# Kernel tuning notes

Measured on AMD Instinct MI355X. Metric: run time of the kernel, lower is better.

Reference implementation:

```python
import jax, jax.numpy as jnp
import numpy as np

NUM_HEADS = 8
LN_EPS = 1e-5


def setup_inputs() -> dict:
    key = jax.random.key(0)
    ks = jax.random.split(key, 9)
    B, C, H, W = 8, 512, 32, 32
    s = 1.0 / np.sqrt(C)
    return {
        "f_curr": jax.random.normal(ks[0], (B, C, H, W), dtype=jnp.float32),
        "f_prev": jax.random.normal(ks[1], (B, C, H, W), dtype=jnp.float32),
        "f_next": jax.random.normal(ks[2], (B, C, H, W), dtype=jnp.float32),
        "Wq": jax.random.normal(ks[3], (C, C), dtype=jnp.float32) * s,
        "Wk": jax.random.normal(ks[4], (C, C), dtype=jnp.float32) * s,
        "Wv": jax.random.normal(ks[5], (C, C), dtype=jnp.float32) * s,
        "Wo": jax.random.normal(ks[6], (C, C), dtype=jnp.float32) * s,
        "gamma": jnp.ones((C,), dtype=jnp.float32),
        "beta": jnp.zeros((C,), dtype=jnp.float32),
    }


def _flatten(f):
    # [B,C,H,W] -> [B, H*W, C]
    B, C, H, W = f.shape
    return f.reshape(B, C, H * W).transpose(0, 2, 1)


def reference(f_curr, f_prev, f_next, Wq, Wk, Wv, Wo, gamma, beta):
    B, C, H, W = f_curr.shape
    N = H * W
    hd = C // NUM_HEADS
    scale = hd ** -0.5

    curr_flat = _flatten(f_curr)                              # [B,N,C]
    neigh_flat = jnp.concatenate([_flatten(f_prev), _flatten(f_next)], axis=1)  # [B,2N,C]

    # torch Linear (no bias): y = x @ W.T
    Q = curr_flat @ Wq.T                                      # [B,N,C]
    K = neigh_flat @ Wk.T                                     # [B,2N,C]
    V = neigh_flat @ Wv.T                                     # [B,2N,C]

    def split_heads(t, L):
        return t.reshape(B, L, NUM_HEADS, hd).transpose(0, 2, 1, 3)  # [B,h,L,hd]

    Qh = split_heads(Q, N)
    Kh = split_heads(K, 2 * N)
    Vh = split_heads(V, 2 * N)

    scores = jnp.einsum("bhnd,bhmd->bhnm", Qh, Kh) * scale    # [B,h,N,2N]
    attn = jax.nn.softmax(scores, axis=-1)
    out = jnp.einsum("bhnm,bhmd->bhnd", attn, Vh)             # [B,h,N,hd]

    out = out.transpose(0, 2, 1, 3).reshape(B, N, C)          # merge heads
    out = curr_flat + out @ Wo.T                              # residual

    # LayerNorm over channel dim
    mu = jnp.mean(out, axis=-1, keepdims=True)
    var = jnp.mean(jnp.square(out - mu), axis=-1, keepdims=True)
    out = (out - mu) * jax.lax.rsqrt(var + LN_EPS) * gamma + beta

    return out.transpose(0, 2, 1).reshape(B, C, H, W)
```

## Files before the change

kernel.cpp:

```cpp
#include <hip/hip_runtime.h>
#include <hip/hip_bf16.h>
#include <math.h>

#define NH 8
#define HD 64
#define CH 512
#define NT 1024
#define NB 8

typedef __bf16 bf16_t;
typedef bf16_t bf16x8 __attribute__((ext_vector_type(8)));
typedef bf16_t bf16x4 __attribute__((ext_vector_type(4)));
typedef float  f32x4  __attribute__((ext_vector_type(4)));
typedef float  f32x16 __attribute__((ext_vector_type(16)));

#define MFMA16(a, b, c) __builtin_amdgcn_mfma_f32_16x16x32_bf16((a), (b), (c), 0, 0, 0)
#define MFMA32(a, b, c) __builtin_amdgcn_mfma_f32_32x32x16_bf16((a), (b), (c), 0, 0, 0)

__device__ __forceinline__ void gload16(const void* g, void* l) {
    __builtin_amdgcn_global_load_lds(
        (const __attribute__((address_space(1))) void*)g,
        (__attribute__((address_space(3))) void*)l, 16, 0, 0);
}

__global__ __launch_bounds__(256) void prep_kernel(
    const float* __restrict__ fc, const float* __restrict__ fp,
    const float* __restrict__ fn, bf16_t* __restrict__ Xc,
    bf16_t* __restrict__ Xn)
{
    __shared__ __align__(16) bf16_t tile[64 * 64];
    const int t = threadIdx.x;
    const int y = blockIdx.y;
    const int b = y / 3, ft = y % 3;
    const int c0 = (blockIdx.x & 7) * 64;
    const int n0 = (blockIdx.x >> 3) * 64;

    const float* src; bf16_t* dst;
    if (ft == 0)      { src = fc + (size_t)b * CH * NT; dst = Xc + (size_t)b * NT * CH; }
    else if (ft == 1) { src = fp + (size_t)b * CH * NT; dst = Xn + (size_t)b * 2 * NT * CH; }
    else              { src = fn + (size_t)b * CH * NT; dst = Xn + (size_t)b * 2 * NT * CH + (size_t)NT * CH; }

    const int nb = t & 15, cb = t >> 4;
    float4 ld[4];
#pragma unroll
    for (int i = 0; i < 4; ++i)
        ld[i] = *(const float4*)(src + (size_t)(c0 + cb * 4 + i) * NT + n0 + nb * 4);
    const float* lf = (const float*)ld;
#pragma unroll
    for (int j = 0; j < 4; ++j) {
        int n = nb * 4 + j;
        int v = (n >> 2) & 14;
        bf16x4 wv = { (bf16_t)lf[0 * 4 + j], (bf16_t)lf[1 * 4 + j],
                      (bf16_t)lf[2 * 4 + j], (bf16_t)lf[3 * 4 + j] };
        *(bf16x4*)(tile + n * 64 + ((cb ^ v) * 4)) = wv;
    }
    __syncthreads();
#pragma unroll
    for (int i = 0; i < 2; ++i) {
        int gid = t + i * 256;
        int n = gid >> 3, c16 = gid & 7;
        int v = (n >> 2) & 14;
        bf16x8 val = *(const bf16x8*)(tile + n * 64 + (((2 * c16) ^ v) * 4));
        *(bf16x8*)(dst + (size_t)(n0 + n) * CH + c0 + c16 * 8) = val;
    }
}

__global__ __launch_bounds__(256) void wcvt_kernel(
    const float* __restrict__ Wq, const float* __restrict__ Wk,
    const float* __restrict__ Wv, const float* __restrict__ Wo,
    bf16_t* __restrict__ Wb)
{
    const int m = blockIdx.y;
    const float* src = (m == 0) ? Wq : (m == 1) ? Wk : (m == 2) ? Wv : Wo;
    bf16_t* dst = Wb + (size_t)m * CH * CH;
    int gid = blockIdx.x * 256 + threadIdx.x;
    float4 v = *(const float4*)(src + (size_t)gid * 4);
    bf16x4 o = { (bf16_t)v.x, (bf16_t)v.y, (bf16_t)v.z, (bf16_t)v.w };
    *(bf16x4*)(dst + (size_t)gid * 4) = o;
}

template <bool SWAP>
__device__ __forceinline__ void gemm_core(const bf16_t* __restrict__ A,
                                          const bf16_t* __restrict__ B,
                                          bf16_t* aT, bf16_t* bT,
                                          f32x4 acc[4][4])
{
    const int t = threadIdx.x, w = t >> 6, lane = t & 63;
    const int lid = lane & 15, quad = lane >> 4;
    const int wm = w >> 1, wn = w & 1;
    const int l4 = lane >> 2, k4 = lane & 3;

    for (int kt = 0; kt < 16; ++kt) {
        const int k0 = kt * 32;
        __syncthreads();
#pragma unroll
        for (int i = 0; i < 2; ++i) {
            int q = w * 2 + i;
            int row = q * 16 + l4;
            int kk = k4 ^ ((row >> 1) & 3);
            gload16(A + (size_t)row * CH + k0 + kk * 8, aT + q * 512);
            gload16(B + (size_t)row * CH + k0 + kk * 8, bT + q * 512);
        }
        __syncthreads();

        const bf16_t* mT = SWAP ? bT : aT;
        const bf16_t* nT = SWAP ? aT : bT;
        bf16x8 mf[4], nf[4];
#pragma unroll
        for (int i = 0; i < 4; ++i) {
            int row = wm * 64 + i * 16 + lid;
            int kw = quad ^ ((row >> 1) & 3);
            mf[i] = *(const bf16x8*)(mT + row * 32 + kw * 8);
        }
#pragma unroll
        for (int i = 0; i < 4; ++i) {
            int row = wn * 64 + i * 16 + lid;
            int kw = quad ^ ((row >> 1) & 3);
            nf[i] = *(const bf16x8*)(nT + row * 32 + kw * 8);
        }
#pragma unroll
        for (int mi = 0; mi < 4; ++mi)
#pragma unroll
            for (int ni = 0; ni < 4; ++ni)
                acc[mi][ni] = MFMA16(mf[mi], nf[ni], acc[mi][ni]);
    }
}

__global__ __launch_bounds__(256) void qkv_kernel(
    const bf16_t* __restrict__ Xc, const bf16_t* __restrict__ Xn,
    const bf16_t* __restrict__ Wb,
    bf16_t* __restrict__ Qn, bf16_t* __restrict__ Kn, bf16_t* __restrict__ Vt)
{
    __shared__ __align__(16) bf16_t aT[128 * 32];
    __shared__ __align__(16) bf16_t bT[128 * 32];
    const int bx = blockIdx.x, b = blockIdx.y;
    const int t = threadIdx.x, w = t >> 6, lane = t & 63;
    const int lid = lane & 15, quad = lane >> 4;
    const int wm = w >> 1, wn = w & 1;
    const float QSC = 0.125f * 1.44269504f;

    f32x4 acc[4][4] = {};

    if (bx < 96) {
        const bf16_t* A; const bf16_t* B; bf16_t* O; float scale;
        if (bx < 32) {
            int nt = bx >> 2, ct = bx & 3;
            A = Xc + (size_t)b * NT * CH + (size_t)nt * 128 * CH;
            B = Wb + (size_t)0 * CH * CH + (size_t)ct * 128 * CH;
            O = Qn + (size_t)b * NT * CH + (size_t)nt * 128 * CH + ct * 128;
            scale = QSC;
        } else {
            int j = bx - 32, nt = j >> 2, ct = j & 3;
            A = Xn + (size_t)b * 2 * NT * CH + (size_t)nt * 128 * CH;
            B = Wb + (size_t)1 * CH * CH + (size_t)ct * 128 * CH;
            O = Kn + (size_t)b * 2 * NT * CH + (size_t)nt * 128 * CH + ct * 128;
            scale = 1.0f;
        }
        gemm_core<false>(A, B, aT, bT, acc);
#pragma unroll
        for (int mi = 0; mi < 4; ++mi)
#pragma unroll
            for (int ni = 0; ni < 4; ++ni)
#pragma unroll
                for (int r = 0; r < 4; ++r) {
                    int n  = wm * 64 + mi * 16 + quad * 4 + r;
                    int co = wn * 64 + ni * 16 + lid;
                    O[(size_t)n * CH + co] = (bf16_t)(acc[mi][ni][r] * scale);
                }
    } else {
        int j = bx - 96, nt = j >> 2, ct = j & 3;
        const bf16_t* A = Xn + (size_t)b * 2 * NT * CH + (size_t)nt * 128 * CH;
        const bf16_t* B = Wb + (size_t)2 * CH * CH + (size_t)ct * 128 * CH;
        bf16_t* O = Vt + (size_t)b * CH * 2 * NT + (size_t)ct * 128 * 2 * NT + nt * 128;
        gemm_core<true>(A, B, aT, bT, acc);
#pragma unroll
        for (int mi = 0; mi < 4; ++mi)
#pragma unroll
            for (int ni = 0; ni < 4; ++ni)
#pragma unroll
                for (int r = 0; r < 4; ++r) {
                    int co_l  = wm * 64 + mi * 16 + quad * 4 + r;
                    int key_l = wn * 64 + ni * 16 + lid;
                    O[(size_t)co_l * (2 * NT) + key_l] = (bf16_t)acc[mi][ni][r];
                }
    }
}

__global__ __launch_bounds__(256) void attn_kernel(
    const bf16_t* __restrict__ Qn, const bf16_t* __restrict__ Kn,
    const bf16_t* __restrict__ Vt, bf16_t* __restrict__ AOn)
{
    __shared__ __align__(16) bf16_t kv[128 * 72];
    __shared__ __align__(16) float  pqf[9216];
    __shared__ float l_scr[128];

    bf16_t* pq = (bf16_t*)pqf;

    const int t = threadIdx.x;
    const int w = t >> 6, lane = t & 63;
    const int wq = w >> 1, wk = w & 1;
    const int l31 = lane & 31, h = lane >> 5;

    const int q0 = blockIdx.x * 128;
    const int hh = blockIdx.y, b = blockIdx.z;

    const bf16_t* Qb  = Qn + ((size_t)b * NT + q0) * CH + hh * HD;
    const bf16_t* Kb  = Kn + (size_t)b * 2 * NT * CH + hh * HD;
    const bf16_t* Vtb = Vt + ((size_t)b * CH + hh * HD) * (2 * NT);
    bf16_t* AOb = AOn + ((size_t)b * NT + q0) * CH + hh * HD;

#pragma unroll
    for (int i = 0; i < 4; ++i) {
        int gid = t + i * 256;
        int qr = gid >> 3, c8 = (gid & 7) * 8;
        *(bf16x8*)(pq + qr * 72 + (c8 ^ (qr & 24))) =
            *(const bf16x8*)(Qb + (size_t)qr * CH + c8);
    }
    __syncthreads();

    bf16x8 kreg[4];
#pragma unroll
    for (int i = 0; i < 4; ++i) {
        int gid = t + i * 256;
        int kr = gid >> 3, c8 = (gid & 7) * 8;
        kreg[i] = *(const bf16x8*)(Kb + (size_t)kr * CH + c8);
    }

    bf16x8 qf[2][4];
#pragma unroll
    for (int nf = 0; nf < 2; ++nf)
#pragma unroll
        for (int ks = 0; ks < 4; ++ks) {
            int row = wq * 64 + nf * 32 + l31;
            int col = (ks * 16 + h * 8) ^ (row & 24);
            qf[nf][ks] = *(const bf16x8*)(pq + row * 72 + col);
        }
    __syncthreads();

    bf16_t* pw = pq + w * 4608;

    f32x16 o[2][2] = {};
    float lpart[2] = {0.f, 0.f};

    for (int kt = 0; kt < 16; ++kt) {
        const int kbase = kt * 128;

#pragma unroll
        for (int i = 0; i < 4; ++i) {
            int gid = t + i * 256;
            int kr = gid >> 3, c8 = (gid & 7) * 8;
            *(bf16x8*)(kv + kr * 72 + (c8 ^ (kr & 24))) = kreg[i];
        }
        __syncthreads();

        bf16x8 vreg[4];
#pragma unroll
        for (int i = 0; i < 4; ++i) {
            int gid = t + i * 256;
            int dr = gid >> 4, c8 = (gid & 15) * 8;
            vreg[i] = *(const bf16x8*)(Vtb + (size_t)dr * (2 * NT) + kbase + c8);
        }

        f32x16 s[2][2] = {};
#pragma unroll
        for (int ks = 0; ks < 4; ++ks) {
            bf16x8 af[2];
#pragma unroll
            for (int mf = 0; mf < 2; ++mf) {
                int arow = wk * 64 + mf * 32 + l31;
                int acol = (ks * 16 + h * 8) ^ (arow & 24);
                af[mf] = *(const bf16x8*)(kv + arow * 72 + acol);
            }
#pragma unroll
            for (int mf = 0; mf < 2; ++mf)
#pragma unroll
                for (int nf = 0; nf < 2; ++nf)
                    s[mf][nf] = MFMA32(af[mf], qf[nf][ks], s[mf][nf]);
        }

#pragma unroll
        for (int mf = 0; mf < 2; ++mf)
#pragma unroll
            for (int nf = 0; nf < 2; ++nf) {
                int qrow = nf * 32 + l31;
#pragma unroll
                for (int g = 0; g < 4; ++g) {
                    float p0 = exp2f(s[mf][nf][4 * g + 0]);
                    float p1 = exp2f(s[mf][nf][4 * g + 1]);
                    float p2 = exp2f(s[mf][nf][4 * g + 2]);
                    float p3 = exp2f(s[mf][nf][4 * g + 3]);
                    lpart[nf] += (p0 + p1) + (p2 + p3);
                    bf16x4 pk = { (bf16_t)p0, (bf16_t)p1, (bf16_t)p2, (bf16_t)p3 };
                    int kb = mf * 32 + 8 * g + 4 * h;
                    *(bf16x4*)(pw + qrow * 72 + (kb ^ (qrow & 24))) = pk;
                }
            }
        __syncthreads();

#pragma unroll
        for (int i = 0; i < 4; ++i) {
            int gid = t + i * 256;
            int dr = gid >> 4, c8 = (gid & 15) * 8;
            *(bf16x8*)(kv + dr * 136 + (c8 ^ (dr & 24))) = vreg[i];
        }
        __syncthreads();

        const int nb2 = (kt < 15) ? kbase + 128 : kbase;
#pragma unroll
        for (int i = 0; i < 4; ++i) {
            int gid = t + i * 256;
            int kr = gid >> 3, c8 = (gid & 7) * 8;
            kreg[i] = *(const bf16x8*)(Kb + (size_t)(nb2 + kr) * CH + c8);
        }

#pragma unroll
        for (int ks = 0; ks < 4; ++ks) {
            bf16x8 av[2], bp[2];
#pragma unroll
            for (int df = 0; df < 2; ++df) {
                int vrow = df * 32 + l31;
                int vcol = (wk * 64 + ks * 16 + h * 8) ^ (vrow & 24);
                av[df] = *(const bf16x8*)(kv + vrow * 136 + vcol);
            }
#pragma unroll
            for (int nf = 0; nf < 2; ++nf) {
                int bq = nf * 32 + l31;
                int bcol = (ks * 16 + h * 8) ^ (bq & 24);
                bp[nf] = *(const bf16x8*)(pw + bq * 72 + bcol);
            }
#pragma unroll
            for (int df = 0; df < 2; ++df)
#pragma unroll
                for (int nf = 0; nf < 2; ++nf)
                    o[df][nf] = MFMA32(av[df], bp[nf], o[df][nf]);
        }
        __syncthreads();
    }

    float l2[2];
#pragma unroll
    for (int nf = 0; nf < 2; ++nf)
        l2[nf] = lpart[nf] + __shfl_xor(lpart[nf], 32);

    if (wk == 1) {
        float* scr = pqf + wq * 4352;
#pragma unroll
        for (int df = 0; df < 2; ++df)
#pragma unroll
            for (int nf = 0; nf < 2; ++nf) {
                int qrow = nf * 32 + l31;
#pragma unroll
                for (int g = 0; g < 4; ++g) {
                    int d = df * 32 + 8 * g + 4 * h;
                    f32x4 v = { o[df][nf][4 * g + 0], o[df][nf][4 * g + 1],
                                o[df][nf][4 * g + 2], o[df][nf][4 * g + 3] };
                    *(f32x4*)(scr + qrow * 68 + d) = v;
                }
            }
        if (h == 0) {
            l_scr[wq * 64 + 0 * 32 + l31] = l2[0];
            l_scr[wq * 64 + 1 * 32 + l31] = l2[1];
        }
    }
    __syncthreads();

    if (wk == 0) {
        const float* scr = pqf + wq * 4352;
        float inv[2];
#pragma unroll
        for (int nf = 0; nf < 2; ++nf)
            inv[nf] = 1.0f / (l2[nf] + l_scr[wq * 64 + nf * 32 + l31]);
#pragma unroll
        for (int df = 0; df < 2; ++df)
#pragma unroll
            for (int nf = 0; nf < 2; ++nf) {
                int qrow = nf * 32 + l31;
#pragma unroll
                for (int g = 0; g < 4; ++g) {
                    int d = df * 32 + 8 * g + 4 * h;
                    f32x4 part = *(const f32x4*)(scr + qrow * 68 + d);
                    bf16x4 ov = {
                        (bf16_t)((o[df][nf][4 * g + 0] + part.x) * inv[nf]),
                        (bf16_t)((o[df][nf][4 * g + 1] + part.y) * inv[nf]),
                        (bf16_t)((o[df][nf][4 * g + 2] + part.z) * inv[nf]),
                        (bf16_t)((o[df][nf][4 * g + 3] + part.w) * inv[nf]) };
                    int qg = wq * 64 + qrow;
                    *(bf16x4*)(kv + qg * 72 + (d ^ (qg & 24))) = ov;
                }
            }
    }
    __syncthreads();

#pragma unroll
    for (int i = 0; i < 4; ++i) {
        int gid = t + i * 256;
        int qr = gid >> 3, c8 = (gid & 7) * 8;
        *(bf16x8*)(AOb + (size_t)qr * CH + c8) =
            *(const bf16x8*)(kv + qr * 72 + (c8 ^ (qr & 24)));
    }
}

__global__ __launch_bounds__(256) void proj_kernel(
    const bf16_t* __restrict__ AOn, const bf16_t* __restrict__ Wb,
    const float* __restrict__ fc, float* __restrict__ Zt)
{
    __shared__ __align__(16) bf16_t aT[128 * 32];
    __shared__ __align__(16) bf16_t bT[128 * 32];
    const int bx = blockIdx.x, b = blockIdx.y;
    const int nt = bx >> 2, ct = bx & 3;
    const int t = threadIdx.x, w = t >> 6, lane = t & 63;
    const int lid = lane & 15, quad = lane >> 4;
    const int wm = w >> 1, wn = w & 1;

    const bf16_t* A = AOn + (size_t)b * NT * CH + (size_t)nt * 128 * CH;
    const bf16_t* B = Wb + (size_t)3 * CH * CH + (size_t)ct * 128 * CH;

    f32x4 acc[4][4] = {};
    gemm_core<true>(A, B, aT, bT, acc);

    const size_t bofs = (size_t)b * CH * NT;
#pragma unroll
    for (int mi = 0; mi < 4; ++mi)
#pragma unroll
        for (int ni = 0; ni < 4; ++ni)
#pragma unroll
            for (int r = 0; r < 4; ++r) {
                int co_l = wm * 64 + mi * 16 + quad * 4 + r;
                int n_l  = wn * 64 + ni * 16 + lid;
                size_t idx = bofs + (size_t)(ct * 128 + co_l) * NT + nt * 128 + n_l;
                Zt[idx] = acc[mi][ni][r] + fc[idx];
            }
}

__global__ __launch_bounds__(256) void stats_kernel(
    const float* __restrict__ Zt, float* __restrict__ mu_buf,
    float* __restrict__ rs_buf)
{
    __shared__ float sS[1024], sQ[1024];
    const int b = blockIdx.y, n0 = blockIdx.x * 64;
    const int t = threadIdx.x, w = t >> 6, lane = t & 63;
    const int co_off = lane >> 4, n4 = lane & 15;
    const float* Zb = Zt + (size_t)b * CH * NT + n0 + n4 * 4;

    f32x4 s = {0, 0, 0, 0}, q = {0, 0, 0, 0};
    for (int it = 0; it < 32; ++it) {
        int co = w * 4 + co_off + it * 16;
        f32x4 z = *(const f32x4*)(Zb + (size_t)co * NT);
#pragma unroll
        for (int c = 0; c < 4; ++c) { s[c] += z[c]; q[c] += z[c] * z[c]; }
    }
#pragma unroll
    for (int c = 0; c < 4; ++c) { sS[t * 4 + c] = s[c]; sQ[t * 4 + c] = q[c]; }
    __syncthreads();

    if (t < 64) {
        int n4r = t >> 2, comp = t & 3;
        float ss = 0.f, qq = 0.f;
#pragma unroll
        for (int i = 0; i < 16; ++i) {
            int idx = ((i >> 2) * 64 + (i & 3) * 16 + n4r) * 4 + comp;
            ss += sS[idx]; qq += sQ[idx];
        }
        float mu  = ss * (1.0f / 512.0f);
        float var = qq * (1.0f / 512.0f) - mu * mu;
        mu_buf[(size_t)b * NT + n0 + t] = mu;
        rs_buf[(size_t)b * NT + n0 + t] = rsqrtf(var + 1e-5f);
    }
}

__global__ __launch_bounds__(256) void apply_kernel(
    const float* __restrict__ Zt, const float* __restrict__ mu_buf,
    const float* __restrict__ rs_buf, const float* __restrict__ gamma,
    const float* __restrict__ beta, float* __restrict__ out)
{
    const int row = blockIdx.x;
    const int co = row & 511, b = row >> 9;
    const int t = threadIdx.x;
    const float g = gamma[co], be = beta[co];
    const size_t base = (size_t)row * NT + t * 4;
    f32x4 z  = *(const f32x4*)(Zt + base);
    f32x4 mu = *(const f32x4*)(mu_buf + (size_t)b * NT + t * 4);
    f32x4 rs = *(const f32x4*)(rs_buf + (size_t)b * NT + t * 4);
    f32x4 o;
#pragma unroll
    for (int c = 0; c < 4; ++c) o[c] = (z[c] - mu[c]) * rs[c] * g + be;
    *(f32x4*)(out + base) = o;
}

extern "C" void kernel_launch(void* const* d_in, const int* in_sizes, int n_in,
                              void* d_out, int out_size, void* d_ws, size_t ws_size,
                              hipStream_t stream)
{
    (void)in_sizes; (void)n_in; (void)out_size; (void)ws_size;
    const float* fc    = (const float*)d_in[0];
    const float* fp    = (const float*)d_in[1];
    const float* fn    = (const float*)d_in[2];
    const float* Wq    = (const float*)d_in[3];
    const float* Wk    = (const float*)d_in[4];
    const float* Wv    = (const float*)d_in[5];
    const float* Wo    = (const float*)d_in[6];
    const float* gamma = (const float*)d_in[7];
    const float* beta  = (const float*)d_in[8];
    float* out = (float*)d_out;

    char* ws = (char*)d_ws;
    bf16_t* Xn  = (bf16_t*)(ws);
    bf16_t* Qn  = (bf16_t*)(ws + 16777216);
    bf16_t* Kn  = (bf16_t*)(ws + 25165824);
    bf16_t* Xc  = (bf16_t*)(ws + 41943040);
    bf16_t* AOn = Xc;
    bf16_t* Vt  = (bf16_t*)(ws + 50331648);
    bf16_t* Wb  = (bf16_t*)(ws + 67108864);
    float*  mu  = (float*)(ws + 69206016);
    float*  rs  = (float*)(ws + 69238784);
    float*  Zt  = (float*)(ws);

    prep_kernel<<<dim3(128, 24), 256, 0, stream>>>(fc, fp, fn, Xc, Xn);
    wcvt_kernel<<<dim3(256, 4), 256, 0, stream>>>(Wq, Wk, Wv, Wo, Wb);
    qkv_kernel<<<dim3(160, 8), 256, 0, stream>>>(Xc, Xn, Wb, Qn, Kn, Vt);
    attn_kernel<<<dim3(8, 8, 8), 256, 0, stream>>>(Qn, Kn, Vt, AOn);
    proj_kernel<<<dim3(32, 8), 256, 0, stream>>>(AOn, Wb, fc, Zt);
    stats_kernel<<<dim3(16, 8), 256, 0, stream>>>(Zt, mu, rs);
    apply_kernel<<<4096, 256, 0, stream>>>(Zt, mu, rs, gamma, beta, out);
}
```

Measured before the change: 252.9 us.

## Restructure attention K/V staging, use raw exp, fuse LayerNorm stats and apply

The attention kernel now gives K and V their own LDS buffers. Both are prefetched one tile ahead into registers and stored together, which cuts the per-iteration barriers from four to two. The XOR swizzle is replaced with an additive skew, and exp2f is replaced by an inline v_exp_f32 to avoid range-handling code. The separate stats and apply kernels are merged into one LayerNorm kernel that reads Zt twice but skips the mu/rs round trip and one launch. The fused LN kernel uses only 128 blocks with scalar strided loads, so it may use bandwidth poorly. The extra LDS buffer may also lower attention occupancy.

```diff
diff --git a/kernel.cpp b/kernel.cpp
--- a/kernel.cpp
+++ b/kernel.cpp
@@ -17,10 +17,18 @@
 #define MFMA16(a, b, c) __builtin_amdgcn_mfma_f32_16x16x32_bf16((a), (b), (c), 0, 0, 0)
 #define MFMA32(a, b, c) __builtin_amdgcn_mfma_f32_32x32x16_bf16((a), (b), (c), 0, 0, 0)
 
+#define SKW(r) (((r) >> 2) & 6)
+
 __device__ __forceinline__ void gload16(const void* g, void* l) {
     __builtin_amdgcn_global_load_lds(
         (const __attribute__((address_space(1))) void*)g,
         (__attribute__((address_space(3))) void*)l, 16, 0, 0);
+}
+
+__device__ __forceinline__ float fexp2(float x) {
+    float r;
+    asm("v_exp_f32 %0, %1" : "=v"(r) : "v"(x));
+    return r;
 }
 
 __global__ __launch_bounds__(256) void prep_kernel(
@@ -190,10 +198,10 @@
     const bf16_t* __restrict__ Qn, const bf16_t* __restrict__ Kn,
     const bf16_t* __restrict__ Vt, bf16_t* __restrict__ AOn)
 {
-    __shared__ __align__(16) bf16_t kv[128 * 72];
+    __shared__ __align__(16) bf16_t k_lds[128 * 72];
+    __shared__ __align__(16) bf16_t v_lds[64 * 136];
     __shared__ __align__(16) float  pqf[9216];
     __shared__ float l_scr[128];
-
     bf16_t* pq = (bf16_t*)pqf;
 
     const int t = threadIdx.x;
@@ -209,22 +217,16 @@
     const bf16_t* Vtb = Vt + ((size_t)b * CH + hh * HD) * (2 * NT);
     bf16_t* AOb = AOn + ((size_t)b * NT + q0) * CH + hh * HD;
 
-#pragma unroll
-    for (int i = 0; i < 4; ++i) {
-        int gid = t + i * 256;
-        int qr = gid >> 3, c8 = (gid & 7) * 8;
-        *(bf16x8*)(pq + qr * 72 + (c8 ^ (qr & 24))) =
-            *(const bf16x8*)(Qb + (size_t)qr * CH + c8);
-    }
-    __syncthreads();
-
-    bf16x8 kreg[4];
-#pragma unroll
-    for (int i = 0; i < 4; ++i) {
-        int gid = t + i * 256;
-        int kr = gid >> 3, c8 = (gid & 7) * 8;
-        kreg[i] = *(const bf16x8*)(Kb + (size_t)kr * CH + c8);
-    }
+    {
+        int qr = t >> 3, c8 = (t & 7) * 8;
+#pragma unroll
+        for (int i = 0; i < 4; ++i) {
+            int row = qr + i * 32;
+            *(bf16x8*)(pq + row * 72 + c8 + SKW(row)) =
+                *(const bf16x8*)(Qb + (size_t)row * CH + c8);
+        }
+    }
+    __syncthreads();
 
     bf16x8 qf[2][4];
 #pragma unroll
@@ -232,33 +234,47 @@
 #pragma unroll
         for (int ks = 0; ks < 4; ++ks) {
             int row = wq * 64 + nf * 32 + l31;
-            int col = (ks * 16 + h * 8) ^ (row & 24);
-            qf[nf][ks] = *(const bf16x8*)(pq + row * 72 + col);
+            qf[nf][ks] = *(const bf16x8*)(pq + row * 72 + ks * 16 + h * 8 + SKW(row));
         }
     __syncthreads();
 
     bf16_t* pw = pq + w * 4608;
+
+    const int kr0 = t >> 3, kc8 = (t & 7) * 8;
+    const int dr0 = t >> 4, vc8 = (t & 15) * 8;
+    const bf16_t* kg = Kb + (size_t)kr0 * CH + kc8;
+    const bf16_t* vg = Vtb + (size_t)dr0 * (2 * NT) + vc8;
+
+    bf16x8 kreg[4], vreg[4];
+#pragma unroll
+    for (int i = 0; i < 4; ++i) kreg[i] = *(const bf16x8*)(kg + (size_t)i * 32 * CH);
+#pragma unroll
+    for (int i = 0; i < 4; ++i) vreg[i] = *(const bf16x8*)(vg + (size_t)i * 16 * (2 * NT));
+    kg += (size_t)128 * CH; vg += 128;
 
     f32x16 o[2][2] = {};
     float lpart[2] = {0.f, 0.f};
 
     for (int kt = 0; kt < 16; ++kt) {
-        const int kbase = kt * 128;
-
+        __syncthreads();
 #pragma unroll
         for (int i = 0; i < 4; ++i) {
-            int gid = t + i * 256;
-            int kr = gid >> 3, c8 = (gid & 7) * 8;
-            *(bf16x8*)(kv + kr * 72 + (c8 ^ (kr & 24))) = kreg[i];
+            int row = kr0 + i * 32;
+            *(bf16x8*)(k_lds + row * 72 + kc8 + SKW(row)) = kreg[i];
+        }
+#pragma unroll
+        for (int i = 0; i < 4; ++i) {
+            int row = dr0 + i * 16;
+            *(bf16x8*)(v_lds + row * 136 + vc8 + SKW(row)) = vreg[i];
         }
         __syncthreads();
 
-        bf16x8 vreg[4];
-#pragma unroll
-        for (int i = 0; i < 4; ++i) {
-            int gid = t + i * 256;
-            int dr = gid >> 4, c8 = (gid & 15) * 8;
-            vreg[i] = *(const bf16x8*)(Vtb + (size_t)dr * (2 * NT) + kbase + c8);
+        if (kt != 15) {
+#pragma unroll
+            for (int i = 0; i < 4; ++i) kreg[i] = *(const bf16x8*)(kg + (size_t)i * 32 * CH);
+#pragma unroll
+            for (int i = 0; i < 4; ++i) vreg[i] = *(const bf16x8*)(vg + (size_t)i * 16 * (2 * NT));
+            kg += (size_t)128 * CH; vg += 128;
         }
 
         f32x16 s[2][2] = {};
@@ -268,8 +284,7 @@
 #pragma unroll
             for (int mf = 0; mf < 2; ++mf) {
                 int arow = wk * 64 + mf * 32 + l31;
-                int acol = (ks * 16 + h * 8) ^ (arow & 24);
-                af[mf] = *(const bf16x8*)(kv + arow * 72 + acol);
+                af[mf] = *(const bf16x8*)(k_lds + arow * 72 + ks * 16 + h * 8 + SKW(arow));
             }
 #pragma unroll
             for (int mf = 0; mf < 2; ++mf)
@@ -285,33 +300,16 @@
                 int qrow = nf * 32 + l31;
 #pragma unroll
                 for (int g = 0; g < 4; ++g) {
-                    float p0 = exp2f(s[mf][nf][4 * g + 0]);
-                    float p1 = exp2f(s[mf][nf][4 * g + 1]);
-                    float p2 = exp2f(s[mf][nf][4 * g + 2]);
-                    float p3 = exp2f(s[mf][nf][4 * g + 3]);
+                    float p0 = fexp2(s[mf][nf][4 * g + 0]);
+                    float p1 = fexp2(s[mf][nf][4 * g + 1]);
+                    float p2 = fexp2(s[mf][nf][4 * g + 2]);
+                    float p3 = fexp2(s[mf][nf][4 * g + 3]);
                     lpart[nf] += (p0 + p1) + (p2 + p3);
                     bf16x4 pk = { (bf16_t)p0, (bf16_t)p1, (bf16_t)p2, (bf16_t)p3 };
                     int kb = mf * 32 + 8 * g + 4 * h;
-                    *(bf16x4*)(pw + qrow * 72 + (kb ^ (qrow & 24))) = pk;
+                    *(bf16x4*)(pw + qrow * 72 + kb + SKW(qrow)) = pk;
                 }
             }
-        __syncthreads();
-
-#pragma unroll
-        for (int i = 0; i < 4; ++i) {
-            int gid = t + i * 256;
-            int dr = gid >> 4, c8 = (gid & 15) * 8;
-            *(bf16x8*)(kv + dr * 136 + (c8 ^ (dr & 24))) = vreg[i];
-        }
-        __syncthreads();
-
-        const int nb2 = (kt < 15) ? kbase + 128 : kbase;
-#pragma unroll
-        for (int i = 0; i < 4; ++i) {
-            int gid = t + i * 256;
-            int kr = gid >> 3, c8 = (gid & 7) * 8;
-            kreg[i] = *(const bf16x8*)(Kb + (size_t)(nb2 + kr) * CH + c8);
-        }
 
 #pragma unroll
         for (int ks = 0; ks < 4; ++ks) {
@@ -319,14 +317,12 @@
 #pragma unroll
             for (int df = 0; df < 2; ++df) {
                 int vrow = df * 32 + l31;
-                int vcol = (wk * 64 + ks * 16 + h * 8) ^ (vrow & 24);
-                av[df] = *(const bf16x8*)(kv + vrow * 136 + vcol);
+                av[df] = *(const bf16x8*)(v_lds + vrow * 136 + wk * 64 + ks * 16 + h * 8 + SKW(vrow));
             }
 #pragma unroll
             for (int nf = 0; nf < 2; ++nf) {
                 int bq = nf * 32 + l31;
-                int bcol = (ks * 16 + h * 8) ^ (bq & 24);
-                bp[nf] = *(const bf16x8*)(pw + bq * 72 + bcol);
+                bp[nf] = *(const bf16x8*)(pw + bq * 72 + ks * 16 + h * 8 + SKW(bq));
             }
 #pragma unroll
             for (int df = 0; df < 2; ++df)
@@ -334,8 +330,8 @@
                 for (int nf = 0; nf < 2; ++nf)
                     o[df][nf] = MFMA32(av[df], bp[nf], o[df][nf]);
         }
-        __syncthreads();
-    }
+    }
+    __syncthreads();
 
     float l2[2];
 #pragma unroll
@@ -385,18 +381,20 @@
                         (bf16_t)((o[df][nf][4 * g + 2] + part.z) * inv[nf]),
                         (bf16_t)((o[df][nf][4 * g + 3] + part.w) * inv[nf]) };
                     int qg = wq * 64 + qrow;
-                    *(bf16x4*)(kv + qg * 72 + (d ^ (qg & 24))) = ov;
+                    *(bf16x4*)(k_lds + qg * 72 + d + SKW(qg)) = ov;
                 }
             }
     }
     __syncthreads();
 
-#pragma unroll
-    for (int i = 0; i < 4; ++i) {
-        int gid = t + i * 256;
-        int qr = gid >> 3, c8 = (gid & 7) * 8;
-        *(bf16x8*)(AOb + (size_t)qr * CH + c8) =
-            *(const bf16x8*)(kv + qr * 72 + (c8 ^ (qr & 24)));
+    {
+        int qr = t >> 3, c8 = (t & 7) * 8;
+#pragma unroll
+        for (int i = 0; i < 4; ++i) {
+            int row = qr + i * 32;
+            *(bf16x8*)(AOb + (size_t)row * CH + c8) =
+                *(const bf16x8*)(k_lds + row * 72 + c8 + SKW(row));
+        }
     }
 }
 
@@ -432,59 +430,45 @@
             }
 }
 
-__global__ __launch_bounds__(256) void stats_kernel(
-    const float* __restrict__ Zt, float* __restrict__ mu_buf,
-    float* __restrict__ rs_buf)
-{
-    __shared__ float sS[1024], sQ[1024];
+__global__ __launch_bounds__(256) void ln2_kernel(
+    const float* __restrict__ Zt, const float* __restrict__ gamma,
+    const float* __restrict__ beta, float* __restrict__ out)
+{
+    __shared__ float pS[256], pQ[256];
+    __shared__ float mu_s[64], rs_s[64];
     const int b = blockIdx.y, n0 = blockIdx.x * 64;
-    const int t = threadIdx.x, w = t >> 6, lane = t & 63;
-    const int co_off = lane >> 4, n4 = lane & 15;
-    const float* Zb = Zt + (size_t)b * CH * NT + n0 + n4 * 4;
-
-    f32x4 s = {0, 0, 0, 0}, q = {0, 0, 0, 0};
-    for (int it = 0; it < 32; ++it) {
-        int co = w * 4 + co_off + it * 16;
-        f32x4 z = *(const f32x4*)(Zb + (size_t)co * NT);
-#pragma unroll
-        for (int c = 0; c < 4; ++c) { s[c] += z[c]; q[c] += z[c] * z[c]; }
-    }
-#pragma unroll
-    for (int c = 0; c < 4; ++c) { sS[t * 4 + c] = s[c]; sQ[t * 4 + c] = q[c]; }
-    __syncthreads();
-
+    const int t = threadIdx.x;
+    const int n = t & 63, cg = t >> 6;
+    const float* Zb = Zt + (size_t)b * CH * NT + n0 + n;
+
+    float s = 0.f, q = 0.f;
+#pragma unroll 8
+    for (int k = 0; k < 128; ++k) {
+        int co = cg * 128 + k;
+        float z = Zb[(size_t)co * NT];
+        s += z; q += z * z;
+    }
+    pS[cg * 64 + n] = s; pQ[cg * 64 + n] = q;
+    __syncthreads();
     if (t < 64) {
-        int n4r = t >> 2, comp = t & 3;
         float ss = 0.f, qq = 0.f;
 #pragma unroll
-        for (int i = 0; i < 16; ++i) {
-            int idx = ((i >> 2) * 64 + (i & 3) * 16 + n4r) * 4 + comp;
-            ss += sS[idx]; qq += sQ[idx];
-        }
+        for (int i = 0; i < 4; ++i) { ss += pS[i * 64 + t]; qq += pQ[i * 64 + t]; }
         float mu  = ss * (1.0f / 512.0f);
         float var = qq * (1.0f / 512.0f) - mu * mu;
-        mu_buf[(size_t)b * NT + n0 + t] = mu;
-        rs_buf[(size_t)b * NT + n0 + t] = rsqrtf(var + 1e-5f);
-    }
-}
-
-__global__ __launch_bounds__(256) void apply_kernel(
-    const float* __restrict__ Zt, const float* __restrict__ mu_buf,
-    const float* __restrict__ rs_buf, const float* __restrict__ gamma,
-    const float* __restrict__ beta, float* __restrict__ out)
-{
-    const int row = blockIdx.x;
-    const int co = row & 511, b = row >> 9;
-    const int t = threadIdx.x;
-    const float g = gamma[co], be = beta[co];
-    const size_t base = (size_t)row * NT + t * 4;
-    f32x4 z  = *(const f32x4*)(Zt + base);
-    f32x4 mu = *(const f32x4*)(mu_buf + (size_t)b * NT + t * 4);
-    f32x4 rs = *(const f32x4*)(rs_buf + (size_t)b * NT + t * 4);
-    f32x4 o;
-#pragma unroll
-    for (int c = 0; c < 4; ++c) o[c] = (z[c] - mu[c]) * rs[c] * g + be;
-    *(f32x4*)(out + base) = o;
+        mu_s[t] = mu;
+        rs_s[t] = rsqrtf(var + 1e-5f);
+    }
+    __syncthreads();
+
+    const float mu = mu_s[n], rs = rs_s[n];
+    float* ob = out + (size_t)b * CH * NT + n0 + n;
+#pragma unroll 8
+    for (int k = 0; k < 128; ++k) {
+        int co = cg * 128 + k;
+        float z = Zb[(size_t)co * NT];
+        ob[(size_t)co * NT] = (z - mu) * rs * gamma[co] + beta[co];
+    }
 }
 
 extern "C" void kernel_launch(void* const* d_in, const int* in_sizes, int n_in,
@@ -511,8 +495,6 @@
     bf16_t* AOn = Xc;
     bf16_t* Vt  = (bf16_t*)(ws + 50331648);
     bf16_t* Wb  = (bf16_t*)(ws + 67108864);
-    float*  mu  = (float*)(ws + 69206016);
-    float*  rs  = (float*)(ws + 69238784);
     float*  Zt  = (float*)(ws);
 
     prep_kernel<<<dim3(128, 24), 256, 0, stream>>>(fc, fp, fn, Xc, Xn);
@@ -520,6 +502,5 @@
     qkv_kernel<<<dim3(160, 8), 256, 0, stream>>>(Xc, Xn, Wb, Qn, Kn, Vt);
     attn_kernel<<<dim3(8, 8, 8), 256, 0, stream>>>(Qn, Kn, Vt, AOn);
     proj_kernel<<<dim3(32, 8), 256, 0, stream>>>(AOn, Wb, fc, Zt);
-    stats_kernel<<<dim3(16, 8), 256, 0, stream>>>(Zt, mu, rs);
-    apply_kernel<<<4096, 256, 0, stream>>>(Zt, mu, rs, gamma, beta, out);
-}
+    ln2_kernel<<<dim3(16, 8), 256, 0, stream>>>(Zt, gamma, beta, out);
+}
```

Measured after the change: 311.3 us. 23.1% more time.

## Widen GEMM tiles to 128x256 and fuse LayerNorm stats with apply

Applied to the files above, without the earlier changes.

The QKV and output-projection GEMMs now use 128x256 tiles, so each block loads a wider slice of the weight matrix and keeps 32 accumulators per thread. This halves the block count and the re-reads of activation tiles. The separate LayerNorm stats and apply kernels are merged into one kernel that computes per-position mean and rstd, then normalizes in a second pass over the same Zt columns. This removes a launch and the mu/rs round trip. The trade-offs are more register pressure, fewer blocks (128 for proj, 128 for LN) leaving many CUs idle on a 256-CU part, and scalar strided loads in the LN kernel.

```diff
diff --git a/kernel.cpp b/kernel.cpp
--- a/kernel.cpp
+++ b/kernel.cpp
@@ -80,11 +80,13 @@
 }
 
 template <bool SWAP>
-__device__ __forceinline__ void gemm_core(const bf16_t* __restrict__ A,
-                                          const bf16_t* __restrict__ B,
-                                          bf16_t* aT, bf16_t* bT,
-                                          f32x4 acc[4][4])
-{
+__device__ __forceinline__ void gemm_core2(const bf16_t* __restrict__ A,
+                                           const bf16_t* __restrict__ B,
+                                           bf16_t* aT, bf16_t* bT,
+                                           f32x4* acc)
+{
+    constexpr int MC = SWAP ? 8 : 4;
+    constexpr int NC = SWAP ? 4 : 8;
     const int t = threadIdx.x, w = t >> 6, lane = t & 63;
     const int lid = lane & 15, quad = lane >> 4;
     const int wm = w >> 1, wn = w & 1;
@@ -99,30 +101,36 @@
             int row = q * 16 + l4;
             int kk = k4 ^ ((row >> 1) & 3);
             gload16(A + (size_t)row * CH + k0 + kk * 8, aT + q * 512);
+        }
+#pragma unroll
+        for (int i = 0; i < 4; ++i) {
+            int q = w * 4 + i;
+            int row = q * 16 + l4;
+            int kk = k4 ^ ((row >> 1) & 3);
             gload16(B + (size_t)row * CH + k0 + kk * 8, bT + q * 512);
         }
         __syncthreads();
 
         const bf16_t* mT = SWAP ? bT : aT;
         const bf16_t* nT = SWAP ? aT : bT;
-        bf16x8 mf[4], nf[4];
-#pragma unroll
-        for (int i = 0; i < 4; ++i) {
-            int row = wm * 64 + i * 16 + lid;
+        bf16x8 mf[MC], nf[NC];
+#pragma unroll
+        for (int i = 0; i < MC; ++i) {
+            int row = wm * (MC * 16) + i * 16 + lid;
             int kw = quad ^ ((row >> 1) & 3);
             mf[i] = *(const bf16x8*)(mT + row * 32 + kw * 8);
         }
 #pragma unroll
-        for (int i = 0; i < 4; ++i) {
-            int row = wn * 64 + i * 16 + lid;
+        for (int i = 0; i < NC; ++i) {
+            int row = wn * (NC * 16) + i * 16 + lid;
             int kw = quad ^ ((row >> 1) & 3);
             nf[i] = *(const bf16x8*)(nT + row * 32 + kw * 8);
         }
 #pragma unroll
-        for (int mi = 0; mi < 4; ++mi)
-#pragma unroll
-            for (int ni = 0; ni < 4; ++ni)
-                acc[mi][ni] = MFMA16(mf[mi], nf[ni], acc[mi][ni]);
+        for (int mi = 0; mi < MC; ++mi)
+#pragma unroll
+            for (int ni = 0; ni < NC; ++ni)
+                acc[mi * NC + ni] = MFMA16(mf[mi], nf[ni], acc[mi * NC + ni]);
     }
 }
 
@@ -132,56 +140,58 @@
     bf16_t* __restrict__ Qn, bf16_t* __restrict__ Kn, bf16_t* __restrict__ Vt)
 {
     __shared__ __align__(16) bf16_t aT[128 * 32];
-    __shared__ __align__(16) bf16_t bT[128 * 32];
+    __shared__ __align__(16) bf16_t bT[256 * 32];
     const int bx = blockIdx.x, b = blockIdx.y;
     const int t = threadIdx.x, w = t >> 6, lane = t & 63;
     const int lid = lane & 15, quad = lane >> 4;
     const int wm = w >> 1, wn = w & 1;
     const float QSC = 0.125f * 1.44269504f;
 
-    f32x4 acc[4][4] = {};
-
-    if (bx < 96) {
+    f32x4 acc[32];
+#pragma unroll
+    for (int i = 0; i < 32; ++i) acc[i] = f32x4{0.f, 0.f, 0.f, 0.f};
+
+    if (bx < 48) {
         const bf16_t* A; const bf16_t* B; bf16_t* O; float scale;
-        if (bx < 32) {
-            int nt = bx >> 2, ct = bx & 3;
+        if (bx < 16) {
+            int nt = bx >> 1, cp = bx & 1;
             A = Xc + (size_t)b * NT * CH + (size_t)nt * 128 * CH;
-            B = Wb + (size_t)0 * CH * CH + (size_t)ct * 128 * CH;
-            O = Qn + (size_t)b * NT * CH + (size_t)nt * 128 * CH + ct * 128;
+            B = Wb + (size_t)0 * CH * CH + (size_t)cp * 256 * CH;
+            O = Qn + (size_t)b * NT * CH + (size_t)nt * 128 * CH + cp * 256;
             scale = QSC;
         } else {
-            int j = bx - 32, nt = j >> 2, ct = j & 3;
+            int j = bx - 16, nt = j >> 1, cp = j & 1;
             A = Xn + (size_t)b * 2 * NT * CH + (size_t)nt * 128 * CH;
-            B = Wb + (size_t)1 * CH * CH + (size_t)ct * 128 * CH;
-            O = Kn + (size_t)b * 2 * NT * CH + (size_t)nt * 128 * CH + ct * 128;
+            B = Wb + (size_t)1 * CH * CH + (size_t)cp * 256 * CH;
+            O = Kn + (size_t)b * 2 * NT * CH + (size_t)nt * 128 * CH + cp * 256;
             scale = 1.0f;
         }
-        gemm_core<false>(A, B, aT, bT, acc);
+        gemm_core2<false>(A, B, aT, bT, acc);
 #pragma unroll
         for (int mi = 0; mi < 4; ++mi)
 #pragma unroll
-            for (int ni = 0; ni < 4; ++ni)
+            for (int ni = 0; ni < 8; ++ni)
 #pragma unroll
                 for (int r = 0; r < 4; ++r) {
                     int n  = wm * 64 + mi * 16 + quad * 4 + r;
-                    int co = wn * 64 + ni * 16 + lid;
-                    O[(size_t)n * CH + co] = (bf16_t)(acc[mi][ni][r] * scale);
+                    int co = wn * 128 + ni * 16 + lid;
+                    O[(size_t)n * CH + co] = (bf16_t)(acc[mi * 8 + ni][r] * scale);
                 }
     } else {
-        int j = bx - 96, nt = j >> 2, ct = j & 3;
+        int j = bx - 48, nt = j >> 1, cp = j & 1;
         const bf16_t* A = Xn + (size_t)b * 2 * NT * CH + (size_t)nt * 128 * CH;
-        const bf16_t* B = Wb + (size_t)2 * CH * CH + (size_t)ct * 128 * CH;
-        bf16_t* O = Vt + (size_t)b * CH * 2 * NT + (size_t)ct * 128 * 2 * NT + nt * 128;
-        gemm_core<true>(A, B, aT, bT, acc);
-#pragma unroll
-        for (int mi = 0; mi < 4; ++mi)
+        const bf16_t* B = Wb + (size_t)2 * CH * CH + (size_t)cp * 256 * CH;
+        bf16_t* O = Vt + (size_t)b * CH * 2 * NT + (size_t)cp * 256 * 2 * NT + nt * 128;
+        gemm_core2<true>(A, B, aT, bT, acc);
+#pragma unroll
+        for (int mi = 0; mi < 8; ++mi)
 #pragma unroll
             for (int ni = 0; ni < 4; ++ni)
 #pragma unroll
                 for (int r = 0; r < 4; ++r) {
-                    int co_l  = wm * 64 + mi * 16 + quad * 4 + r;
+                    int co_l  = wm * 128 + mi * 16 + quad * 4 + r;
                     int key_l = wn * 64 + ni * 16 + lid;
-                    O[(size_t)co_l * (2 * NT) + key_l] = (bf16_t)acc[mi][ni][r];
+                    O[(size_t)co_l * (2 * NT) + key_l] = (bf16_t)acc[mi * 4 + ni][r];
                 }
     }
 }
@@ -405,86 +415,74 @@
     const float* __restrict__ fc, float* __restrict__ Zt)
 {
     __shared__ __align__(16) bf16_t aT[128 * 32];
-    __shared__ __align__(16) bf16_t bT[128 * 32];
+    __shared__ __align__(16) bf16_t bT[256 * 32];
     const int bx = blockIdx.x, b = blockIdx.y;
-    const int nt = bx >> 2, ct = bx & 3;
+    const int nt = bx >> 1, cp = bx & 1;
     const int t = threadIdx.x, w = t >> 6, lane = t & 63;
     const int lid = lane & 15, quad = lane >> 4;
     const int wm = w >> 1, wn = w & 1;
 
     const bf16_t* A = AOn + (size_t)b * NT * CH + (size_t)nt * 128 * CH;
-    const bf16_t* B = Wb + (size_t)3 * CH * CH + (size_t)ct * 128 * CH;
-
-    f32x4 acc[4][4] = {};
-    gemm_core<true>(A, B, aT, bT, acc);
+    const bf16_t* B = Wb + (size_t)3 * CH * CH + (size_t)cp * 256 * CH;
+
+    f32x4 acc[32];
+#pragma unroll
+    for (int i = 0; i < 32; ++i) acc[i] = f32x4{0.f, 0.f, 0.f, 0.f};
+    gemm_core2<true>(A, B, aT, bT, acc);
 
     const size_t bofs = (size_t)b * CH * NT;
 #pragma unroll
-    for (int mi = 0; mi < 4; ++mi)
+    for (int mi = 0; mi < 8; ++mi)
 #pragma unroll
         for (int ni = 0; ni < 4; ++ni)
 #pragma unroll
             for (int r = 0; r < 4; ++r) {
-                int co_l = wm * 64 + mi * 16 + quad * 4 + r;
+                int co_l = wm * 128 + mi * 16 + quad * 4 + r;
                 int n_l  = wn * 64 + ni * 16 + lid;
-                size_t idx = bofs + (size_t)(ct * 128 + co_l) * NT + nt * 128 + n_l;
-                Zt[idx] = acc[mi][ni][r] + fc[idx];
-            }
-}
-
-__global__ __launch_bounds__(256) void stats_kernel(
-    const float* __restrict__ Zt, float* __restrict__ mu_buf,
-    float* __restrict__ rs_buf)
-{
-    __shared__ float sS[1024], sQ[1024];
+                size_t idx = bofs + (size_t)(cp * 256 + co_l) * NT + nt * 128 + n_l;
+                Zt[idx] = acc[mi * 4 + ni][r] + fc[idx];
+            }
+}
+
+__global__ __launch_bounds__(256) void ln2_kernel(
+    const float* __restrict__ Zt, const float* __restrict__ gamma,
+    const float* __restrict__ beta, float* __restrict__ out)
+{
+    __shared__ float pS[256], pQ[256];
+    __shared__ float mu_s[64], rs_s[64];
     const int b = blockIdx.y, n0 = blockIdx.x * 64;
-    const int t = threadIdx.x, w = t >> 6, lane = t & 63;
-    const int co_off = lane >> 4, n4 = lane & 15;
-    const float* Zb = Zt + (size_t)b * CH * NT + n0 + n4 * 4;
-
-    f32x4 s = {0, 0, 0, 0}, q = {0, 0, 0, 0};
-    for (int it = 0; it < 32; ++it) {
-        int co = w * 4 + co_off + it * 16;
-        f32x4 z = *(const f32x4*)(Zb + (size_t)co * NT);
-#pragma unroll
-        for (int c = 0; c < 4; ++c) { s[c] += z[c]; q[c] += z[c] * z[c]; }
-    }
-#pragma unroll
-    for (int c = 0; c < 4; ++c) { sS[t * 4 + c] = s[c]; sQ[t * 4 + c] = q[c]; }
-    __syncthreads();
-
+    const int t = threadIdx.x;
+    const int n = t & 63, cg = t >> 6;
+    const float* Zb = Zt + (size_t)b * CH * NT + n0 + n;
+
+    float s = 0.f, q = 0.f;
+#pragma unroll 8
+    for (int k = 0; k < 128; ++k) {
+        int co = cg * 128 + k;
+        float z = Zb[(size_t)co * NT];
+        s += z; q += z * z;
+    }
+    pS[cg * 64 + n] = s; pQ[cg * 64 + n] = q;
+    __syncthreads();
     if (t < 64) {
-        int n4r = t >> 2, comp = t & 3;
         float ss = 0.f, qq = 0.f;
 #pragma unroll
-        for (int i = 0; i < 16; ++i) {
-            int idx = ((i >> 2) * 64 + (i & 3) * 16 + n4r) * 4 + comp;
-            ss += sS[idx]; qq += sQ[idx];
-        }
+        for (int i = 0; i < 4; ++i) { ss += pS[i * 64 + t]; qq += pQ[i * 64 + t]; }
         float mu  = ss * (1.0f / 512.0f);
         float var = qq * (1.0f / 512.0f) - mu * mu;
-        mu_buf[(size_t)b * NT + n0 + t] = mu;
-        rs_buf[(size_t)b * NT + n0 + t] = rsqrtf(var + 1e-5f);
-    }
-}
-
-__global__ __launch_bounds__(256) void apply_kernel(
-    const float* __restrict__ Zt, const float* __restrict__ mu_buf,
-    const float* __restrict__ rs_buf, const float* __restrict__ gamma,
-    const float* __restrict__ beta, float* __restrict__ out)
-{
-    const int row = blockIdx.x;
-    const int co = row & 511, b = row >> 9;
-    const int t = threadIdx.x;
-    const float g = gamma[co], be = beta[co];
-    const size_t base = (size_t)row * NT + t * 4;
-    f32x4 z  = *(const f32x4*)(Zt + base);
-    f32x4 mu = *(const f32x4*)(mu_buf + (size_t)b * NT + t * 4);
-    f32x4 rs = *(const f32x4*)(rs_buf + (size_t)b * NT + t * 4);
-    f32x4 o;
-#pragma unroll
-    for (int c = 0; c < 4; ++c) o[c] = (z[c] - mu[c]) * rs[c] * g + be;
-    *(f32x4*)(out + base) = o;
+        mu_s[t] = mu;
+        rs_s[t] = rsqrtf(var + 1e-5f);
+    }
+    __syncthreads();
+
+    const float mu = mu_s[n], rs = rs_s[n];
+    float* ob = out + (size_t)b * CH * NT + n0 + n;
+#pragma unroll 8
+    for (int k = 0; k < 128; ++k) {
+        int co = cg * 128 + k;
+        float z = Zb[(size_t)co * NT];
+        ob[(size_t)co * NT] = (z - mu) * rs * gamma[co] + beta[co];
+    }
 }
 
 extern "C" void kernel_launch(void* const* d_in, const int* in_sizes, int n_in,
@@ -511,15 +509,12 @@
     bf16_t* AOn = Xc;
     bf16_t* Vt  = (bf16_t*)(ws + 50331648);
     bf16_t* Wb  = (bf16_t*)(ws + 67108864);
-    float*  mu  = (float*)(ws + 69206016);
-    float*  rs  = (float*)(ws + 69238784);
     float*  Zt  = (float*)(ws);
 
     prep_kernel<<<dim3(128, 24), 256, 0, stream>>>(fc, fp, fn, Xc, Xn);
     wcvt_kernel<<<dim3(256, 4), 256, 0, stream>>>(Wq, Wk, Wv, Wo, Wb);
-    qkv_kernel<<<dim3(160, 8), 256, 0, stream>>>(Xc, Xn, Wb, Qn, Kn, Vt);
+    qkv_kernel<<<dim3(80, 8), 256, 0, stream>>>(Xc, Xn, Wb, Qn, Kn, Vt);
     attn_kernel<<<dim3(8, 8, 8), 256, 0, stream>>>(Qn, Kn, Vt, AOn);
-    proj_kernel<<<dim3(32, 8), 256, 0, stream>>>(AOn, Wb, fc, Zt);
-    stats_kernel<<<dim3(16, 8), 256, 0, stream>>>(Zt, mu, rs);
-    apply_kernel<<<4096, 256, 0, stream>>>(Zt, mu, rs, gamma, beta, out);
-}
+    proj_kernel<<<dim3(16, 8), 256, 0, stream>>>(AOn, Wb, fc, Zt);
+    ln2_kernel<<<dim3(16, 8), 256, 0, stream>>>(Zt, gamma, beta, out);
+}
```

New measurement: 285.3 us. 12.8% more time.

## Keep softmax probabilities in registers and fuse LayerNorm stats with apply

Applied to the files above, without the earlier changes.

In the attention kernel, the exp'd probabilities are no longer written to and reread from LDS. They stay in registers and are rearranged into the MFMA B-operand layout with cross-half-wave shuffles, which removes LDS traffic and bank pressure in the PV step. Separately, the stats and apply LayerNorm kernels are merged into one kernel that computes per-column mean and rstd in shared memory, then normalizes the same 64-column slab. This drops one launch and the mu/rs global round trip, but the merged kernel runs only 128 blocks with scalar strided loads, so it may underuse bandwidth compared with the 4096-block apply kernel.

```diff
diff --git a/kernel.cpp b/kernel.cpp
--- a/kernel.cpp
+++ b/kernel.cpp
@@ -21,6 +21,14 @@
     __builtin_amdgcn_global_load_lds(
         (const __attribute__((address_space(1))) void*)g,
         (__attribute__((address_space(3))) void*)l, 16, 0, 0);
+}
+
+__device__ __forceinline__ bf16x4 shfl32_b4(bf16x4 v) {
+    union { bf16x4 v; int i[2]; } u;
+    u.v = v;
+    u.i[0] = __shfl_xor(u.i[0], 32, 64);
+    u.i[1] = __shfl_xor(u.i[1], 32, 64);
+    return u.v;
 }
 
 __global__ __launch_bounds__(256) void prep_kernel(
@@ -237,8 +245,6 @@
         }
     __syncthreads();
 
-    bf16_t* pw = pq + w * 4608;
-
     f32x16 o[2][2] = {};
     float lpart[2] = {0.f, 0.f};
 
@@ -278,11 +284,11 @@
                     s[mf][nf] = MFMA32(af[mf], qf[nf][ks], s[mf][nf]);
         }
 
+        bf16x4 P4[2][2][4];
 #pragma unroll
         for (int mf = 0; mf < 2; ++mf)
 #pragma unroll
             for (int nf = 0; nf < 2; ++nf) {
-                int qrow = nf * 32 + l31;
 #pragma unroll
                 for (int g = 0; g < 4; ++g) {
                     float p0 = exp2f(s[mf][nf][4 * g + 0]);
@@ -290,9 +296,8 @@
                     float p2 = exp2f(s[mf][nf][4 * g + 2]);
                     float p3 = exp2f(s[mf][nf][4 * g + 3]);
                     lpart[nf] += (p0 + p1) + (p2 + p3);
-                    bf16x4 pk = { (bf16_t)p0, (bf16_t)p1, (bf16_t)p2, (bf16_t)p3 };
-                    int kb = mf * 32 + 8 * g + 4 * h;
-                    *(bf16x4*)(pw + qrow * 72 + (kb ^ (qrow & 24))) = pk;
+                    P4[mf][nf][g] = bf16x4{ (bf16_t)p0, (bf16_t)p1,
+                                            (bf16_t)p2, (bf16_t)p3 };
                 }
             }
         __syncthreads();
@@ -315,7 +320,8 @@
 
 #pragma unroll
         for (int ks = 0; ks < 4; ++ks) {
-            bf16x8 av[2], bp[2];
+            const int mf = ks >> 1, gs = (ks & 1) * 2;
+            bf16x8 av[2];
 #pragma unroll
             for (int df = 0; df < 2; ++df) {
                 int vrow = df * 32 + l31;
@@ -324,15 +330,17 @@
             }
 #pragma unroll
             for (int nf = 0; nf < 2; ++nf) {
-                int bq = nf * 32 + l31;
-                int bcol = (ks * 16 + h * 8) ^ (bq & 24);
-                bp[nf] = *(const bf16x8*)(pw + bq * 72 + bcol);
-            }
-#pragma unroll
-            for (int df = 0; df < 2; ++df)
-#pragma unroll
-                for (int nf = 0; nf < 2; ++nf)
-                    o[df][nf] = MFMA32(av[df], bp[nf], o[df][nf]);
+                bf16x4 own = h ? P4[mf][nf][gs + 1] : P4[mf][nf][gs];
+                bf16x4 snd = h ? P4[mf][nf][gs]     : P4[mf][nf][gs + 1];
+                bf16x4 rcv = shfl32_b4(snd);
+                bf16x4 lo = h ? rcv : own;
+                bf16x4 hi = h ? own : rcv;
+                bf16x8 bp = { lo[0], lo[1], lo[2], lo[3],
+                              hi[0], hi[1], hi[2], hi[3] };
+#pragma unroll
+                for (int df = 0; df < 2; ++df)
+                    o[df][nf] = MFMA32(av[df], bp, o[df][nf]);
+            }
         }
         __syncthreads();
     }
@@ -432,59 +440,45 @@
             }
 }
 
-__global__ __launch_bounds__(256) void stats_kernel(
-    const float* __restrict__ Zt, float* __restrict__ mu_buf,
-    float* __restrict__ rs_buf)
-{
-    __shared__ float sS[1024], sQ[1024];
+__global__ __launch_bounds__(256) void ln2_kernel(
+    const float* __restrict__ Zt, const float* __restrict__ gamma,
+    const float* __restrict__ beta, float* __restrict__ out)
+{
+    __shared__ float pS[256], pQ[256];
+    __shared__ float mu_s[64], rs_s[64];
     const int b = blockIdx.y, n0 = blockIdx.x * 64;
-    const int t = threadIdx.x, w = t >> 6, lane = t & 63;
-    const int co_off = lane >> 4, n4 = lane & 15;
-    const float* Zb = Zt + (size_t)b * CH * NT + n0 + n4 * 4;
-
-    f32x4 s = {0, 0, 0, 0}, q = {0, 0, 0, 0};
-    for (int it = 0; it < 32; ++it) {
-        int co = w * 4 + co_off + it * 16;
-        f32x4 z = *(const f32x4*)(Zb + (size_t)co * NT);
-#pragma unroll
-        for (int c = 0; c < 4; ++c) { s[c] += z[c]; q[c] += z[c] * z[c]; }
-    }
-#pragma unroll
-    for (int c = 0; c < 4; ++c) { sS[t * 4 + c] = s[c]; sQ[t * 4 + c] = q[c]; }
-    __syncthreads();
-
+    const int t = threadIdx.x;
+    const int n = t & 63, cg = t >> 6;
+    const float* Zb = Zt + (size_t)b * CH * NT + n0 + n;
+
+    float s = 0.f, q = 0.f;
+#pragma unroll 8
+    for (int k = 0; k < 128; ++k) {
+        int co = cg * 128 + k;
+        float z = Zb[(size_t)co * NT];
+        s += z; q += z * z;
+    }
+    pS[cg * 64 + n] = s; pQ[cg * 64 + n] = q;
+    __syncthreads();
     if (t < 64) {
-        int n4r = t >> 2, comp = t & 3;
         float ss = 0.f, qq = 0.f;
 #pragma unroll
-        for (int i = 0; i < 16; ++i) {
-            int idx = ((i >> 2) * 64 + (i & 3) * 16 + n4r) * 4 + comp;
-            ss += sS[idx]; qq += sQ[idx];
-        }
+        for (int i = 0; i < 4; ++i) { ss += pS[i * 64 + t]; qq += pQ[i * 64 + t]; }
         float mu  = ss * (1.0f / 512.0f);
         float var = qq * (1.0f / 512.0f) - mu * mu;
-        mu_buf[(size_t)b * NT + n0 + t] = mu;
-        rs_buf[(size_t)b * NT + n0 + t] = rsqrtf(var + 1e-5f);
-    }
-}
-
-__global__ __launch_bounds__(256) void apply_kernel(
-    const float* __restrict__ Zt, const float* __restrict__ mu_buf,
-    const float* __restrict__ rs_buf, const float* __restrict__ gamma,
-    const float* __restrict__ beta, float* __restrict__ out)
-{
-    const int row = blockIdx.x;
-    const int co = row & 511, b = row >> 9;
-    const int t = threadIdx.x;
-    const float g = gamma[co], be = beta[co];
-    const size_t base = (size_t)row * NT + t * 4;
-    f32x4 z  = *(const f32x4*)(Zt + base);
-    f32x4 mu = *(const f32x4*)(mu_buf + (size_t)b * NT + t * 4);
-    f32x4 rs = *(const f32x4*)(rs_buf + (size_t)b * NT + t * 4);
-    f32x4 o;
-#pragma unroll
-    for (int c = 0; c < 4; ++c) o[c] = (z[c] - mu[c]) * rs[c] * g + be;
-    *(f32x4*)(out + base) = o;
+        mu_s[t] = mu;
+        rs_s[t] = rsqrtf(var + 1e-5f);
+    }
+    __syncthreads();
+
+    const float mu = mu_s[n], rs = rs_s[n];
+    float* ob = out + (size_t)b * CH * NT + n0 + n;
+#pragma unroll 8
+    for (int k = 0; k < 128; ++k) {
+        int co = cg * 128 + k;
+        float z = Zb[(size_t)co * NT];
+        ob[(size_t)co * NT] = (z - mu) * rs * gamma[co] + beta[co];
+    }
 }
 
 extern "C" void kernel_launch(void* const* d_in, const int* in_sizes, int n_in,
@@ -511,8 +505,6 @@
     bf16_t* AOn = Xc;
     bf16_t* Vt  = (bf16_t*)(ws + 50331648);
     bf16_t* Wb  = (bf16_t*)(ws + 67108864);
-    float*  mu  = (float*)(ws + 69206016);
-    float*  rs  = (float*)(ws + 69238784);
     float*  Zt  = (float*)(ws);
 
     prep_kernel<<<dim3(128, 24), 256, 0, stream>>>(fc, fp, fn, Xc, Xn);
@@ -520,6 +512,5 @@
     qkv_kernel<<<dim3(160, 8), 256, 0, stream>>>(Xc, Xn, Wb, Qn, Kn, Vt);
     attn_kernel<<<dim3(8, 8, 8), 256, 0, stream>>>(Qn, Kn, Vt, AOn);
     proj_kernel<<<dim3(32, 8), 256, 0, stream>>>(AOn, Wb, fc, Zt);
-    stats_kernel<<<dim3(16, 8), 256, 0, stream>>>(Zt, mu, rs);
-    apply_kernel<<<4096, 256, 0, stream>>>(Zt, mu, rs, gamma, beta, out);
-}
+    ln2_kernel<<<dim3(16, 8), 256, 0, stream>>>(Zt, gamma, beta, out);
+}
```

After: 267.5 us. 5.7% more time.
